# Kernel optimization log

Hardware: AMD Instinct MI355X
Metric: run time of the kernel (lower is better)

Reference implementation:

```python
import jax, jax.numpy as jnp
import numpy as np

N_HEADS = 8
OUT_FEATURES = 64
LEAKY_SLOPE = 0.2
MASK_FILL = -1e9


def setup_inputs() -> dict:
    key = jax.random.key(0)
    k_h, k_adj, k_W, k_a = jax.random.split(key, 4)
    B, N, F_IN = 1, 4096, 128
    h = jax.random.normal(k_h, (B, N, F_IN), dtype=jnp.float32)
    adj_mat = jax.random.randint(k_adj, (N, N), 0, 2, dtype=jnp.int32)
    # glorot-style scaled params
    W = jax.random.normal(k_W, (F_IN, OUT_FEATURES * N_HEADS), dtype=jnp.float32) * (1.0 / np.sqrt(F_IN))
    a = jax.random.normal(k_a, (N_HEADS, 2 * OUT_FEATURES, 1), dtype=jnp.float32) * (1.0 / np.sqrt(2 * OUT_FEATURES))
    return {"h": h, "adj_mat": adj_mat, "W": W, "a": a}


def reference(h, adj_mat, W, a):
    B, N, _ = h.shape
    heads = a.shape[0]
    out = a.shape[1] // 2
    # linear transform + head split (same reshape order as tf.reshape)
    ht = jnp.reshape(h @ W, (-1, heads, N, out))            # (B, heads, N, out)
    # additive attention scores
    src = jnp.einsum('bhnf,hfo->bhno', ht, a[:, :out, :])    # (B, heads, N, 1)
    tgt = jnp.einsum('bhnf,hfo->bhno', ht, a[:, out:, :])    # (B, heads, N, 1)
    e = src + jnp.swapaxes(tgt, -1, -2)                      # (B, heads, N, N)
    e = jnp.where(e > 0, e, LEAKY_SLOPE * e)                 # leaky_relu
    e = jnp.where(adj_mat > 0, e, MASK_FILL)                 # adjacency mask
    attention = jax.nn.softmax(e, axis=-1)
    h_prime = attention @ ht                                 # (B, heads, N, out)
    return h_prime
```

## Files before the change

kernel.cpp:

```cpp
#include <hip/hip_runtime.h>
#include <stdint.h>

#define HT_STRIDE 262144
#define LOG2E 1.4426950408889634f

typedef __attribute__((ext_vector_type(8))) short bf16x8;
typedef __attribute__((ext_vector_type(4))) float f32x4;
typedef __attribute__((ext_vector_type(2))) float f32x2;

__device__ __forceinline__ unsigned short f2bf(float f) {
    unsigned int u = __float_as_uint(f);
    u += 0x7FFFu + ((u >> 16) & 1u);
    return (unsigned short)(u >> 16);
}

__device__ __forceinline__ float exp2_fast(float e) {
#if __has_builtin(__builtin_amdgcn_exp2f)
    return __builtin_amdgcn_exp2f(e);
#else
    return __expf(e * 0.6931471805599453f);
#endif
}

__global__ void __launch_bounds__(256) k_fused(const float* __restrict__ h,
                                               const int* __restrict__ adj,
                                               const float* __restrict__ W,
                                               const float* __restrict__ aW,
                                               float* __restrict__ ess,
                                               float* __restrict__ ets,
                                               unsigned short* __restrict__ htT2,
                                               unsigned int* __restrict__ abm) {
    __shared__ unsigned int ldsT[1024];
    __shared__ float hs[8][128];
    __shared__ float ldsA[64][66];
    __shared__ float redS[4][64];
    __shared__ float redT[4][64];
    const int t = threadIdx.x;

    if (blockIdx.x < 512) {
        const int lane = t & 63;
        const int w = t >> 6;
        const int sb = blockIdx.x >> 3;
        const int cq = blockIdx.x & 7;
        for (int rr = 0; rr < 16; ++rr) {
            const int* arow = adj + (sb * 64 + w * 16 + rr) * 4096 + cq * 512;
            int v[8];
            #pragma unroll
            for (int j = 0; j < 8; ++j) v[j] = arow[j * 64 + lane];
            #pragma unroll
            for (int j = 0; j < 8; ++j) {
                unsigned long long m = __ballot(v[j] > 0);
                if (lane < 2)
                    ldsT[(2 * j + lane) * 64 + rr * 4 + w] = (unsigned int)(m >> (lane * 32));
            }
        }
        __syncthreads();
        ((uint4*)(abm + (sb * 128 + cq * 16) * 64))[t] = ((uint4*)ldsT)[t];
    } else {
        const int bid2 = (int)blockIdx.x - 512;
        const int n0 = bid2 * 8;
        const int p0 = bid2 * 64;
        const int hd = p0 >> 12;
        const int m0 = p0 & 4095;

        {
            float4 v = ((const float4*)(h + n0 * 128))[t];
            int e = t * 4;
            int r = e >> 7, f = e & 127;
            hs[r][f + 0] = v.x; hs[r][f + 1] = v.y;
            hs[r][f + 2] = v.z; hs[r][f + 3] = v.w;
        }
        __syncthreads();

        float acc0[8], acc1[8];
        #pragma unroll
        for (int r = 0; r < 8; ++r) { acc0[r] = 0.f; acc1[r] = 0.f; }
        const float2* Wf = (const float2*)W;
        for (int f = 0; f < 128; ++f) {
            float2 wp = Wf[f * 256 + t];
            #pragma unroll
            for (int r = 0; r < 8; ++r) {
                float hv = hs[r][f];
                acc0[r] = fmaf(hv, wp.x, acc0[r]);
                acc1[r] = fmaf(hv, wp.y, acc1[r]);
            }
        }
        {
            const int ns = t >> 5;
            const int o = (2 * t) & 63;
            #pragma unroll
            for (int r = 0; r < 8; ++r) {
                *(float2*)&ldsA[r * 8 + ns][o] = make_float2(acc0[r], acc1[r]);
            }
        }
        __syncthreads();

        {
            const int r = t & 63, og = t >> 6;
            float sdot = 0.f, gdot = 0.f;
            #pragma unroll
            for (int k = 0; k < 16; ++k) {
                int o = og * 16 + k;
                float hv = ldsA[r][o];
                sdot = fmaf(hv, aW[hd * 128 + o], sdot);
                gdot = fmaf(hv, aW[hd * 128 + 64 + o], gdot);
            }
            redS[og][r] = sdot; redT[og][r] = gdot;
        }
        __syncthreads();
        if (t < 64) {
            float sp = (redS[0][t] + redS[1][t] + redS[2][t] + redS[3][t]) * LOG2E;
            ess[hd * 8192 + m0 + t]        = exp2_fast(sp);
            ess[hd * 8192 + 4096 + m0 + t] = exp2_fast(0.2f * sp);
        } else if (t < 128) {
            int r = t - 64;
            float tv = (redT[0][r] + redT[1][r] + redT[2][r] + redT[3][r]) * LOG2E;
            ets[hd * 8192 + m0 + r]        = exp2_fast(tv);
            ets[hd * 8192 + 4096 + m0 + r] = exp2_fast(0.2f * tv);
        }

        unsigned short* d = htT2 + (hd * 128 + (m0 >> 5)) * 2048;
        #pragma unroll
        for (int i = 0; i < 16; ++i) {
            int id = t + 256 * i;
            int mi = id & 31, o = (id >> 5) & 63, ct = id >> 11;
            d[ct * 2048 + o * 32 + mi] = f2bf(ldsA[mi + 32 * ct][o]);
        }
    }
}

__global__ void __launch_bounds__(256, 4) k_attn(const unsigned int* __restrict__ abm,
                                                 const unsigned short* __restrict__ htT2,
                                                 const float* __restrict__ ess,
                                                 const float* __restrict__ ets,
                                                 float* __restrict__ out) {
    __shared__ __align__(16) float smem[8192];

    const int t = threadIdx.x;
    const int kq = t >> 6;
    const int lane = t & 63;
    const int li = lane & 15;
    const int quad = lane >> 4;
    const int head = blockIdx.x & 7;
    const int s32 = blockIdx.x >> 3;
    const int s64 = s32 >> 1, half = s32 & 1;
    const int i0 = s32 * 32;

    {
        const float4* esrc = (const float4*)(ets + head * 8192);
        float4* edst = (float4*)smem;
        #pragma unroll
        for (int i = 0; i < 8; ++i) edst[t + 256 * i] = esrc[t + 256 * i];
    }

    f32x2 esv[2], es2v[2];
    #pragma unroll
    for (int g2 = 0; g2 < 2; ++g2) {
        float e1 = ess[head * 8192 + i0 + 16 * g2 + li];
        float e2 = ess[head * 8192 + 4096 + i0 + 16 * g2 + li];
        esv[g2]  = (f32x2){e1, e1};
        es2v[g2] = (f32x2){e2, e2};
    }

    f32x4 acc[8];
    #pragma unroll
    for (int i = 0; i < 8; ++i) acc[i] = (f32x4){0.f, 0.f, 0.f, 0.f};
    f32x4 apd[2];
    apd[0] = (f32x4){0.f, 0.f, 0.f, 0.f};
    apd[1] = (f32x4){0.f, 0.f, 0.f, 0.f};

    const uint4 onesw = {0x3F803F80u, 0x3F803F80u, 0x3F803F80u, 0x3F803F80u};
    const bf16x8 aones = __builtin_bit_cast(bf16x8, onesw);

    const uint4* ap = (const uint4*)(htT2 + head * HT_STRIDE) + (li * 4 + quad);
    const unsigned int* bmp = abm + s64 * 8192 + half * 2 + li * 4;

    __syncthreads();

    const int c0 = kq * 32;
    #pragma unroll 1
    for (int ci = 0; ci < 32; ++ci) {
        const int c = c0 + ci;
        uint4 av0 = ap[c * 256 + 0];
        uint4 av1 = ap[c * 256 + 64];
        uint4 av2 = ap[c * 256 + 128];
        uint4 av3 = ap[c * 256 + 192];
        uint2 bw = *(const uint2*)(bmp + c * 64);

        const float4* etp  = (const float4*)(smem + c * 32 + quad * 8);
        const float4* et2p = (const float4*)(smem + 4096 + c * 32 + quad * 8);
        float4 ta = etp[0],  tb = etp[1];
        float4 ua = et2p[0], ub = et2p[1];
        const f32x2 etq[4]  = {(f32x2){ta.x, ta.y}, (f32x2){ta.z, ta.w},
                               (f32x2){tb.x, tb.y}, (f32x2){tb.z, tb.w}};
        const f32x2 et2q[4] = {(f32x2){ua.x, ua.y}, (f32x2){ua.z, ua.w},
                               (f32x2){ub.x, ub.y}, (f32x2){ub.z, ub.w}};

        const unsigned int wb[2] = {bw.x, bw.y};
        #pragma unroll
        for (int g2 = 0; g2 < 2; ++g2) {
            const unsigned int wq = wb[g2] >> (quad * 8);
            unsigned int pk[4];
            #pragma unroll
            for (int m = 0; m < 4; ++m) {
                f32x2 p1 = etq[m] * esv[g2];
                f32x2 p2 = et2q[m] * es2v[g2];
                float w0 = fmaxf(p1[0], p2[0]);
                float w1 = fmaxf(p1[1], p2[1]);
                unsigned int pkm;
                asm("v_cvt_pk_bf16_f32 %0, %1, %2" : "=v"(pkm) : "v"(w0), "v"(w1));
                const int j0 = 2 * m, j1 = 2 * m + 1;
                const unsigned int lo = (unsigned int)((int)(wq << (31 - j0)) >> 31);
                const unsigned int hi = (unsigned int)((int)(wq << (31 - j1)) >> 31);
                pk[m] = pkm & ((lo & 0x0000FFFFu) | (hi & 0xFFFF0000u));
            }
            uint4 bv; bv.x = pk[0]; bv.y = pk[1]; bv.z = pk[2]; bv.w = pk[3];
            bf16x8 bfrag = __builtin_bit_cast(bf16x8, bv);
            apd[g2] = __builtin_amdgcn_mfma_f32_16x16x32_bf16(aones, bfrag, apd[g2], 0, 0, 0);
            acc[g2 * 4 + 0] = __builtin_amdgcn_mfma_f32_16x16x32_bf16(__builtin_bit_cast(bf16x8, av0), bfrag, acc[g2 * 4 + 0], 0, 0, 0);
            acc[g2 * 4 + 1] = __builtin_amdgcn_mfma_f32_16x16x32_bf16(__builtin_bit_cast(bf16x8, av1), bfrag, acc[g2 * 4 + 1], 0, 0, 0);
            acc[g2 * 4 + 2] = __builtin_amdgcn_mfma_f32_16x16x32_bf16(__builtin_bit_cast(bf16x8, av2), bfrag, acc[g2 * 4 + 2], 0, 0, 0);
            acc[g2 * 4 + 3] = __builtin_amdgcn_mfma_f32_16x16x32_bf16(__builtin_bit_cast(bf16x8, av3), bfrag, acc[g2 * 4 + 3], 0, 0, 0);
        }
    }

    __syncthreads();
    if (kq != 0) {
        float* cb = smem + ((kq - 1) * 64 + lane) * 36;
        #pragma unroll
        for (int i = 0; i < 8; ++i) ((f32x4*)cb)[i] = acc[i];
        cb[32] = apd[0][0]; cb[33] = apd[1][0];
    }
    __syncthreads();
    if (kq == 0) {
        float pd[2] = {apd[0][0], apd[1][0]};
        #pragma unroll
        for (int q = 0; q < 3; ++q) {
            const float* cb = smem + (q * 64 + lane) * 36;
            #pragma unroll
            for (int i = 0; i < 8; ++i) acc[i] += ((const f32x4*)cb)[i];
            pd[0] += cb[32]; pd[1] += cb[33];
        }
        #pragma unroll
        for (int g2 = 0; g2 < 2; ++g2) {
            const float rd = 1.0f / pd[g2];
            float4* op = (float4*)(out + head * HT_STRIDE + (i0 + 16 * g2 + li) * 64);
            #pragma unroll
            for (int f = 0; f < 4; ++f) {
                f32x4 a = acc[g2 * 4 + f];
                op[f * 4 + quad] = make_float4(a[0] * rd, a[1] * rd, a[2] * rd, a[3] * rd);
            }
        }
    }
}

extern "C" void kernel_launch(void* const* d_in, const int* in_sizes, int n_in,
                              void* d_out, int out_size, void* d_ws, size_t ws_size,
                              hipStream_t stream) {
    const float* h   = (const float*)d_in[0];
    const int*   adj = (const int*)d_in[1];
    const float* W   = (const float*)d_in[2];
    const float* aW  = (const float*)d_in[3];
    float* out = (float*)d_out;

    char* ws = (char*)d_ws;
    float* ess = (float*)(ws);
    float* ets = (float*)(ws + 262144);
    unsigned int*   abm  = (unsigned int*)(ws + 524288);
    unsigned short* htT2 = (unsigned short*)(ws + 2621440);

    hipLaunchKernelGGL(k_fused, dim3(1024), dim3(256), 0, stream,
                       h, adj, W, aW, ess, ets, htT2, abm);
    hipLaunchKernelGGL(k_attn,  dim3(1024), dim3(256), 0, stream,
                       abm, htT2, ess, ets, out);
}
```

Measured before the change: 150.4 us.

## Widen attention tile to 64 query rows per block to reuse value fragments

Each attention block now handles 64 query rows instead of 32, so every loaded bf16 value fragment feeds twice as many MFMAs. Half as many blocks are launched and per-thread accumulators double, with launch bounds lowered to 2 waves per SIMD and the reduction scratch enlarged. The bit-mask extraction is rewritten with v_bfe_i32 and v_bfi_b32 inline asm, and the loop is unrolled by 2. The trade is fewer blocks in flight and higher register pressure in exchange for half the global traffic on the value matrix.

```diff
diff --git a/kernel.cpp b/kernel.cpp
--- a/kernel.cpp
+++ b/kernel.cpp
@@ -129,12 +129,12 @@
     }
 }
 
-__global__ void __launch_bounds__(256, 4) k_attn(const unsigned int* __restrict__ abm,
+__global__ void __launch_bounds__(256, 2) k_attn(const unsigned int* __restrict__ abm,
                                                  const unsigned short* __restrict__ htT2,
                                                  const float* __restrict__ ess,
                                                  const float* __restrict__ ets,
                                                  float* __restrict__ out) {
-    __shared__ __align__(16) float smem[8192];
+    __shared__ __align__(16) float smem[13056];
 
     const int t = threadIdx.x;
     const int kq = t >> 6;
@@ -142,9 +142,8 @@
     const int li = lane & 15;
     const int quad = lane >> 4;
     const int head = blockIdx.x & 7;
-    const int s32 = blockIdx.x >> 3;
-    const int s64 = s32 >> 1, half = s32 & 1;
-    const int i0 = s32 * 32;
+    const int s64 = blockIdx.x >> 3;
+    const int i0 = s64 * 64;
 
     {
         const float4* esrc = (const float4*)(ets + head * 8192);
@@ -153,39 +152,40 @@
         for (int i = 0; i < 8; ++i) edst[t + 256 * i] = esrc[t + 256 * i];
     }
 
-    f32x2 esv[2], es2v[2];
+    f32x2 esv[4], es2v[4];
     #pragma unroll
-    for (int g2 = 0; g2 < 2; ++g2) {
+    for (int g2 = 0; g2 < 4; ++g2) {
         float e1 = ess[head * 8192 + i0 + 16 * g2 + li];
         float e2 = ess[head * 8192 + 4096 + i0 + 16 * g2 + li];
         esv[g2]  = (f32x2){e1, e1};
         es2v[g2] = (f32x2){e2, e2};
     }
 
-    f32x4 acc[8];
+    f32x4 acc[16];
     #pragma unroll
-    for (int i = 0; i < 8; ++i) acc[i] = (f32x4){0.f, 0.f, 0.f, 0.f};
-    f32x4 apd[2];
-    apd[0] = (f32x4){0.f, 0.f, 0.f, 0.f};
-    apd[1] = (f32x4){0.f, 0.f, 0.f, 0.f};
+    for (int i = 0; i < 16; ++i) acc[i] = (f32x4){0.f, 0.f, 0.f, 0.f};
+    f32x4 apd[4];
+    #pragma unroll
+    for (int g2 = 0; g2 < 4; ++g2) apd[g2] = (f32x4){0.f, 0.f, 0.f, 0.f};
 
     const uint4 onesw = {0x3F803F80u, 0x3F803F80u, 0x3F803F80u, 0x3F803F80u};
     const bf16x8 aones = __builtin_bit_cast(bf16x8, onesw);
-
-    const uint4* ap = (const uint4*)(htT2 + head * HT_STRIDE) + (li * 4 + quad);
-    const unsigned int* bmp = abm + s64 * 8192 + half * 2 + li * 4;
+    const unsigned int lohalf = 0x0000FFFFu;
+
+    const uint4* ap  = (const uint4*)(htT2 + head * HT_STRIDE) + (li * 4 + quad);
+    const uint4* bmp = (const uint4*)(abm + s64 * 8192 + li * 4);
 
     __syncthreads();
 
     const int c0 = kq * 32;
-    #pragma unroll 1
+    #pragma unroll 2
     for (int ci = 0; ci < 32; ++ci) {
         const int c = c0 + ci;
         uint4 av0 = ap[c * 256 + 0];
         uint4 av1 = ap[c * 256 + 64];
         uint4 av2 = ap[c * 256 + 128];
         uint4 av3 = ap[c * 256 + 192];
-        uint2 bw = *(const uint2*)(bmp + c * 64);
+        uint4 bw = bmp[c * 16];
 
         const float4* etp  = (const float4*)(smem + c * 32 + quad * 8);
         const float4* et2p = (const float4*)(smem + 4096 + c * 32 + quad * 8);
@@ -196,9 +196,9 @@
         const f32x2 et2q[4] = {(f32x2){ua.x, ua.y}, (f32x2){ua.z, ua.w},
                                (f32x2){ub.x, ub.y}, (f32x2){ub.z, ub.w}};
 
-        const unsigned int wb[2] = {bw.x, bw.y};
-        #pragma unroll
-        for (int g2 = 0; g2 < 2; ++g2) {
+        const unsigned int wb[4] = {bw.x, bw.y, bw.z, bw.w};
+        #pragma unroll
+        for (int g2 = 0; g2 < 4; ++g2) {
             const unsigned int wq = wb[g2] >> (quad * 8);
             unsigned int pk[4];
             #pragma unroll
@@ -209,10 +209,11 @@
                 float w1 = fmaxf(p1[1], p2[1]);
                 unsigned int pkm;
                 asm("v_cvt_pk_bf16_f32 %0, %1, %2" : "=v"(pkm) : "v"(w0), "v"(w1));
-                const int j0 = 2 * m, j1 = 2 * m + 1;
-                const unsigned int lo = (unsigned int)((int)(wq << (31 - j0)) >> 31);
-                const unsigned int hi = (unsigned int)((int)(wq << (31 - j1)) >> 31);
-                pk[m] = pkm & ((lo & 0x0000FFFFu) | (hi & 0xFFFF0000u));
+                unsigned int lo, hi, msk;
+                asm("v_bfe_i32 %0, %1, %2, 1" : "=v"(lo) : "v"(wq), "n"(2 * m));
+                asm("v_bfe_i32 %0, %1, %2, 1" : "=v"(hi) : "v"(wq), "n"(2 * m + 1));
+                asm("v_bfi_b32 %0, %1, %2, %3" : "=v"(msk) : "v"(lohalf), "v"(lo), "v"(hi));
+                pk[m] = pkm & msk;
             }
             uint4 bv; bv.x = pk[0]; bv.y = pk[1]; bv.z = pk[2]; bv.w = pk[3];
             bf16x8 bfrag = __builtin_bit_cast(bf16x8, bv);
@@ -226,23 +227,25 @@
 
     __syncthreads();
     if (kq != 0) {
-        float* cb = smem + ((kq - 1) * 64 + lane) * 36;
-        #pragma unroll
-        for (int i = 0; i < 8; ++i) ((f32x4*)cb)[i] = acc[i];
-        cb[32] = apd[0][0]; cb[33] = apd[1][0];
+        float* cb = smem + ((kq - 1) * 64 + lane) * 68;
+        #pragma unroll
+        for (int i = 0; i < 16; ++i) ((f32x4*)cb)[i] = acc[i];
+        #pragma unroll
+        for (int g2 = 0; g2 < 4; ++g2) cb[64 + g2] = apd[g2][0];
     }
     __syncthreads();
     if (kq == 0) {
-        float pd[2] = {apd[0][0], apd[1][0]};
+        float pd[4] = {apd[0][0], apd[1][0], apd[2][0], apd[3][0]};
         #pragma unroll
         for (int q = 0; q < 3; ++q) {
-            const float* cb = smem + (q * 64 + lane) * 36;
-            #pragma unroll
-            for (int i = 0; i < 8; ++i) acc[i] += ((const f32x4*)cb)[i];
-            pd[0] += cb[32]; pd[1] += cb[33];
-        }
-        #pragma unroll
-        for (int g2 = 0; g2 < 2; ++g2) {
+            const float* cb = smem + (q * 64 + lane) * 68;
+            #pragma unroll
+            for (int i = 0; i < 16; ++i) acc[i] += ((const f32x4*)cb)[i];
+            #pragma unroll
+            for (int g2 = 0; g2 < 4; ++g2) pd[g2] += cb[64 + g2];
+        }
+        #pragma unroll
+        for (int g2 = 0; g2 < 4; ++g2) {
             const float rd = 1.0f / pd[g2];
             float4* op = (float4*)(out + head * HT_STRIDE + (i0 + 16 * g2 + li) * 64);
             #pragma unroll
@@ -271,6 +274,6 @@
 
     hipLaunchKernelGGL(k_fused, dim3(1024), dim3(256), 0, stream,
                        h, adj, W, aW, ess, ets, htT2, abm);
-    hipLaunchKernelGGL(k_attn,  dim3(1024), dim3(256), 0, stream,
+    hipLaunchKernelGGL(k_attn,  dim3(512),  dim3(256), 0, stream,
                        abm, htT2, ess, ets, out);
 }
```

After: 150.9 us. Within noise of the previous version (+0.4%).

## Split attention row groups across 8 waves, interleave fused blocks, prefetch W

Applied to the files above, without the earlier changes.

The attention kernel now runs 512 threads per block, and each wave handles one 16-row group instead of two. This halves the accumulator registers per wave and doubles the wave count per block, aiming for more latency hiding. The fused prep kernel interleaves adjacency-pack blocks with projection blocks by block-index parity so memory-bound and compute-bound work mix across CUs. The W loads in the projection loop are software-prefetched four rows ahead. In exchange, each htT2 fragment is now loaded by twice as many waves, and the LDS reduction layout changes.

```diff
diff --git a/kernel.cpp b/kernel.cpp
--- a/kernel.cpp
+++ b/kernel.cpp
@@ -37,11 +37,12 @@
     __shared__ float redT[4][64];
     const int t = threadIdx.x;
 
-    if (blockIdx.x < 512) {
+    if ((blockIdx.x & 1) == 0) {
+        const int eid = (int)blockIdx.x >> 1;
         const int lane = t & 63;
         const int w = t >> 6;
-        const int sb = blockIdx.x >> 3;
-        const int cq = blockIdx.x & 7;
+        const int sb = eid >> 3;
+        const int cq = eid & 7;
         for (int rr = 0; rr < 16; ++rr) {
             const int* arow = adj + (sb * 64 + w * 16 + rr) * 4096 + cq * 512;
             int v[8];
@@ -57,7 +58,7 @@
         __syncthreads();
         ((uint4*)(abm + (sb * 128 + cq * 16) * 64))[t] = ((uint4*)ldsT)[t];
     } else {
-        const int bid2 = (int)blockIdx.x - 512;
+        const int bid2 = (int)blockIdx.x >> 1;
         const int n0 = bid2 * 8;
         const int p0 = bid2 * 64;
         const int hd = p0 >> 12;
@@ -76,14 +77,26 @@
         #pragma unroll
         for (int r = 0; r < 8; ++r) { acc0[r] = 0.f; acc1[r] = 0.f; }
         const float2* Wf = (const float2*)W;
-        for (int f = 0; f < 128; ++f) {
-            float2 wp = Wf[f * 256 + t];
-            #pragma unroll
-            for (int r = 0; r < 8; ++r) {
-                float hv = hs[r][f];
-                acc0[r] = fmaf(hv, wp.x, acc0[r]);
-                acc1[r] = fmaf(hv, wp.y, acc1[r]);
-            }
+        float2 wpb[4];
+        #pragma unroll
+        for (int j = 0; j < 4; ++j) wpb[j] = Wf[j * 256 + t];
+        for (int fb = 0; fb < 32; ++fb) {
+            const int fn = ((fb + 1) & 31) * 4;
+            float2 wn[4];
+            #pragma unroll
+            for (int j = 0; j < 4; ++j) wn[j] = Wf[(fn + j) * 256 + t];
+            #pragma unroll
+            for (int j = 0; j < 4; ++j) {
+                const int f = fb * 4 + j;
+                #pragma unroll
+                for (int r = 0; r < 8; ++r) {
+                    float hv = hs[r][f];
+                    acc0[r] = fmaf(hv, wpb[j].x, acc0[r]);
+                    acc1[r] = fmaf(hv, wpb[j].y, acc1[r]);
+                }
+            }
+            #pragma unroll
+            for (int j = 0; j < 4; ++j) wpb[j] = wn[j];
         }
         {
             const int ns = t >> 5;
@@ -129,15 +142,17 @@
     }
 }
 
-__global__ void __launch_bounds__(256, 4) k_attn(const unsigned int* __restrict__ abm,
-                                                 const unsigned short* __restrict__ htT2,
-                                                 const float* __restrict__ ess,
-                                                 const float* __restrict__ ets,
-                                                 float* __restrict__ out) {
+__global__ void __launch_bounds__(512) k_attn(const unsigned int* __restrict__ abm,
+                                              const unsigned short* __restrict__ htT2,
+                                              const float* __restrict__ ess,
+                                              const float* __restrict__ ets,
+                                              float* __restrict__ out) {
     __shared__ __align__(16) float smem[8192];
 
     const int t = threadIdx.x;
-    const int kq = t >> 6;
+    const int wv = t >> 6;
+    const int rh = wv >> 2;
+    const int kq = wv & 3;
     const int lane = t & 63;
     const int li = lane & 15;
     const int quad = lane >> 4;
@@ -150,30 +165,24 @@
         const float4* esrc = (const float4*)(ets + head * 8192);
         float4* edst = (float4*)smem;
         #pragma unroll
-        for (int i = 0; i < 8; ++i) edst[t + 256 * i] = esrc[t + 256 * i];
-    }
-
-    f32x2 esv[2], es2v[2];
+        for (int i = 0; i < 4; ++i) edst[t + 512 * i] = esrc[t + 512 * i];
+    }
+
+    const float e1 = ess[head * 8192 + i0 + 16 * rh + li];
+    const float e2 = ess[head * 8192 + 4096 + i0 + 16 * rh + li];
+    const f32x2 esv  = (f32x2){e1, e1};
+    const f32x2 es2v = (f32x2){e2, e2};
+
+    f32x4 acc[4];
     #pragma unroll
-    for (int g2 = 0; g2 < 2; ++g2) {
-        float e1 = ess[head * 8192 + i0 + 16 * g2 + li];
-        float e2 = ess[head * 8192 + 4096 + i0 + 16 * g2 + li];
-        esv[g2]  = (f32x2){e1, e1};
-        es2v[g2] = (f32x2){e2, e2};
-    }
-
-    f32x4 acc[8];
-    #pragma unroll
-    for (int i = 0; i < 8; ++i) acc[i] = (f32x4){0.f, 0.f, 0.f, 0.f};
-    f32x4 apd[2];
-    apd[0] = (f32x4){0.f, 0.f, 0.f, 0.f};
-    apd[1] = (f32x4){0.f, 0.f, 0.f, 0.f};
+    for (int i = 0; i < 4; ++i) acc[i] = (f32x4){0.f, 0.f, 0.f, 0.f};
+    f32x4 apd = (f32x4){0.f, 0.f, 0.f, 0.f};
 
     const uint4 onesw = {0x3F803F80u, 0x3F803F80u, 0x3F803F80u, 0x3F803F80u};
     const bf16x8 aones = __builtin_bit_cast(bf16x8, onesw);
 
     const uint4* ap = (const uint4*)(htT2 + head * HT_STRIDE) + (li * 4 + quad);
-    const unsigned int* bmp = abm + s64 * 8192 + half * 2 + li * 4;
+    const unsigned int* bmp = abm + s64 * 8192 + li * 4 + half * 2 + rh;
 
     __syncthreads();
 
@@ -185,7 +194,7 @@
         uint4 av1 = ap[c * 256 + 64];
         uint4 av2 = ap[c * 256 + 128];
         uint4 av3 = ap[c * 256 + 192];
-        uint2 bw = *(const uint2*)(bmp + c * 64);
+        const unsigned int bw = bmp[c * 64];
 
         const float4* etp  = (const float4*)(smem + c * 32 + quad * 8);
         const float4* et2p = (const float4*)(smem + 4096 + c * 32 + quad * 8);
@@ -196,60 +205,53 @@
         const f32x2 et2q[4] = {(f32x2){ua.x, ua.y}, (f32x2){ua.z, ua.w},
                                (f32x2){ub.x, ub.y}, (f32x2){ub.z, ub.w}};
 
-        const unsigned int wb[2] = {bw.x, bw.y};
-        #pragma unroll
-        for (int g2 = 0; g2 < 2; ++g2) {
-            const unsigned int wq = wb[g2] >> (quad * 8);
-            unsigned int pk[4];
-            #pragma unroll
-            for (int m = 0; m < 4; ++m) {
-                f32x2 p1 = etq[m] * esv[g2];
-                f32x2 p2 = et2q[m] * es2v[g2];
-                float w0 = fmaxf(p1[0], p2[0]);
-                float w1 = fmaxf(p1[1], p2[1]);
-                unsigned int pkm;
-                asm("v_cvt_pk_bf16_f32 %0, %1, %2" : "=v"(pkm) : "v"(w0), "v"(w1));
-                const int j0 = 2 * m, j1 = 2 * m + 1;
-                const unsigned int lo = (unsigned int)((int)(wq << (31 - j0)) >> 31);
-                const unsigned int hi = (unsigned int)((int)(wq << (31 - j1)) >> 31);
-                pk[m] = pkm & ((lo & 0x0000FFFFu) | (hi & 0xFFFF0000u));
-            }
-            uint4 bv; bv.x = pk[0]; bv.y = pk[1]; bv.z = pk[2]; bv.w = pk[3];
-            bf16x8 bfrag = __builtin_bit_cast(bf16x8, bv);
-            apd[g2] = __builtin_amdgcn_mfma_f32_16x16x32_bf16(aones, bfrag, apd[g2], 0, 0, 0);
-            acc[g2 * 4 + 0] = __builtin_amdgcn_mfma_f32_16x16x32_bf16(__builtin_bit_cast(bf16x8, av0), bfrag, acc[g2 * 4 + 0], 0, 0, 0);
-            acc[g2 * 4 + 1] = __builtin_amdgcn_mfma_f32_16x16x32_bf16(__builtin_bit_cast(bf16x8, av1), bfrag, acc[g2 * 4 + 1], 0, 0, 0);
-            acc[g2 * 4 + 2] = __builtin_amdgcn_mfma_f32_16x16x32_bf16(__builtin_bit_cast(bf16x8, av2), bfrag, acc[g2 * 4 + 2], 0, 0, 0);
-            acc[g2 * 4 + 3] = __builtin_amdgcn_mfma_f32_16x16x32_bf16(__builtin_bit_cast(bf16x8, av3), bfrag, acc[g2 * 4 + 3], 0, 0, 0);
-        }
+        const unsigned int wq = bw >> (quad * 8);
+        unsigned int pk[4];
+        #pragma unroll
+        for (int m = 0; m < 4; ++m) {
+            f32x2 p1 = etq[m] * esv;
+            f32x2 p2 = et2q[m] * es2v;
+            float w0 = fmaxf(p1[0], p2[0]);
+            float w1 = fmaxf(p1[1], p2[1]);
+            unsigned int pkm;
+            asm("v_cvt_pk_bf16_f32 %0, %1, %2" : "=v"(pkm) : "v"(w0), "v"(w1));
+            const int j0 = 2 * m, j1 = 2 * m + 1;
+            const unsigned int lo = (unsigned int)((int)(wq << (31 - j0)) >> 31);
+            const unsigned int hi = (unsigned int)((int)(wq << (31 - j1)) >> 31);
+            pk[m] = pkm & ((lo & 0x0000FFFFu) | (hi & 0xFFFF0000u));
+        }
+        uint4 bv; bv.x = pk[0]; bv.y = pk[1]; bv.z = pk[2]; bv.w = pk[3];
+        bf16x8 bfrag = __builtin_bit_cast(bf16x8, bv);
+        apd    = __builtin_amdgcn_mfma_f32_16x16x32_bf16(aones, bfrag, apd, 0, 0, 0);
+        acc[0] = __builtin_amdgcn_mfma_f32_16x16x32_bf16(__builtin_bit_cast(bf16x8, av0), bfrag, acc[0], 0, 0, 0);
+        acc[1] = __builtin_amdgcn_mfma_f32_16x16x32_bf16(__builtin_bit_cast(bf16x8, av1), bfrag, acc[1], 0, 0, 0);
+        acc[2] = __builtin_amdgcn_mfma_f32_16x16x32_bf16(__builtin_bit_cast(bf16x8, av2), bfrag, acc[2], 0, 0, 0);
+        acc[3] = __builtin_amdgcn_mfma_f32_16x16x32_bf16(__builtin_bit_cast(bf16x8, av3), bfrag, acc[3], 0, 0, 0);
     }
 
     __syncthreads();
     if (kq != 0) {
-        float* cb = smem + ((kq - 1) * 64 + lane) * 36;
-        #pragma unroll
-        for (int i = 0; i < 8; ++i) ((f32x4*)cb)[i] = acc[i];
-        cb[32] = apd[0][0]; cb[33] = apd[1][0];
+        float* cb = smem + ((rh * 3 + (kq - 1)) * 64 + lane) * 20;
+        #pragma unroll
+        for (int i = 0; i < 4; ++i) ((f32x4*)cb)[i] = acc[i];
+        cb[16] = apd[0];
     }
     __syncthreads();
     if (kq == 0) {
-        float pd[2] = {apd[0][0], apd[1][0]};
+        float pd = apd[0];
         #pragma unroll
         for (int q = 0; q < 3; ++q) {
-            const float* cb = smem + (q * 64 + lane) * 36;
-            #pragma unroll
-            for (int i = 0; i < 8; ++i) acc[i] += ((const f32x4*)cb)[i];
-            pd[0] += cb[32]; pd[1] += cb[33];
-        }
-        #pragma unroll
-        for (int g2 = 0; g2 < 2; ++g2) {
-            const float rd = 1.0f / pd[g2];
-            float4* op = (float4*)(out + head * HT_STRIDE + (i0 + 16 * g2 + li) * 64);
-            #pragma unroll
-            for (int f = 0; f < 4; ++f) {
-                f32x4 a = acc[g2 * 4 + f];
-                op[f * 4 + quad] = make_float4(a[0] * rd, a[1] * rd, a[2] * rd, a[3] * rd);
-            }
+            const float* cb = smem + ((rh * 3 + q) * 64 + lane) * 20;
+            #pragma unroll
+            for (int i = 0; i < 4; ++i) acc[i] += ((const f32x4*)cb)[i];
+            pd += cb[16];
+        }
+        const float rd = 1.0f / pd;
+        float4* op = (float4*)(out + head * HT_STRIDE + (i0 + 16 * rh + li) * 64);
+        #pragma unroll
+        for (int f = 0; f < 4; ++f) {
+            f32x4 a = acc[f];
+            op[f * 4 + quad] = make_float4(a[0] * rd, a[1] * rd, a[2] * rd, a[3] * rd);
         }
     }
 }
@@ -271,6 +273,6 @@
 
     hipLaunchKernelGGL(k_fused, dim3(1024), dim3(256), 0, stream,
                        h, adj, W, aW, ess, ets, htT2, abm);
-    hipLaunchKernelGGL(k_attn,  dim3(1024), dim3(256), 0, stream,
+    hipLaunchKernelGGL(k_attn,  dim3(1024), dim3(512), 0, stream,
                        abm, htT2, ess, ets, out);
 }
```

Result: slower. 184.9 us (+22.9%).
